# Performance work log

Measured on AMD Instinct MI355X. Metric: run time of the kernel, lower is better.

Reference implementation:

```python
import jax, jax.numpy as jnp
import numpy as np

B, T, N, F, H, K, E = 4, 256, 48, 4, 64, 4, 192
LH, C = 512, 8
NEG_SLOPE = 0.2


def setup_inputs() -> dict:
    key = jax.random.key(0)
    ks = jax.random.split(key, 16)
    rn = lambda k, shape, s=0.1: jax.random.normal(k, shape, jnp.float32) * s
    x = jax.random.normal(ks[0], (B, T, N, F), jnp.float32)
    edge_index = jax.random.randint(ks[1], (2, E), 0, N, jnp.int32)
    return dict(
        x=x,
        edge_index=edge_index,
        # GATv2 layer 1: F -> K*H, concat heads
        Wl1=rn(ks[2], (F, K * H)), Wr1=rn(ks[3], (F, K * H)),
        att1=rn(ks[4], (K, H)), b1=rn(ks[5], (K * H,)),
        # GATv2 layer 2: K*H -> H, mean over heads
        Wl2=rn(ks[6], (K * H, K * H)), Wr2=rn(ks[7], (K * H, K * H)),
        att2=rn(ks[8], (K, H)), b2=rn(ks[9], (H,)),
        # LSTM (torch gate order i,f,g,o)
        W_ih=rn(ks[10], (4 * LH, N * H), 0.02), W_hh=rn(ks[11], (4 * LH, LH), 0.02),
        b_ih=rn(ks[12], (4 * LH,), 0.02), b_hh=rn(ks[13], (4 * LH,), 0.02),
        fc_w=rn(ks[14], (C, LH)), fc_b=rn(ks[15], (C,)),
    )


def gatv2(xn, src, dst, Wl, Wr, att, bias, concat):
    # xn: [G, N, Fin]; shared edge list src/dst: [E]
    G = xn.shape[0]
    xl = (xn @ Wl).reshape(G, N, K, H)  # source transform (messages)
    xr = (xn @ Wr).reshape(G, N, K, H)  # target transform
    s = jax.nn.leaky_relu(xl[:, src] + xr[:, dst], NEG_SLOPE)  # [G,E,K,H]
    e = jnp.einsum('gekh,kh->gek', s, att)                      # [G,E,K]
    seg_max = jax.vmap(lambda v: jax.ops.segment_max(v, dst, num_segments=N))(e)  # [G,N,K]
    p = jnp.exp(e - seg_max[:, dst])
    denom = jax.vmap(lambda v: jax.ops.segment_sum(v, dst, num_segments=N))(p)
    alpha = p / (denom[:, dst] + 1e-16)                         # softmax over in-edges per node
    msg = alpha[..., None] * xl[:, src]                         # [G,E,K,H]
    out = jax.vmap(lambda m: jax.ops.segment_sum(m, dst, num_segments=N))(msg)  # [G,N,K,H]
    out = out.reshape(G, N, K * H) if concat else out.mean(axis=2)
    return out + bias


def lstm_last(seq, W_ih, W_hh, b_ih, b_hh):
    # seq: [B, T, In] -> last hidden state [B, LH]
    xw = jnp.einsum('bti,gi->btg', seq, W_ih) + (b_ih + b_hh)  # precompute input part
    def step(carry, xt):
        h, c = carry
        g = xt + h @ W_hh.T
        i, f, gg, o = jnp.split(g, 4, axis=-1)
        c = jax.nn.sigmoid(f) * c + jax.nn.sigmoid(i) * jnp.tanh(gg)
        h = jax.nn.sigmoid(o) * jnp.tanh(c)
        return (h, c), None
    h0 = jnp.zeros((seq.shape[0], LH), seq.dtype)
    (h, _c), _ = jax.lax.scan(step, (h0, h0), jnp.swapaxes(xw, 0, 1))
    return h


def reference(x, edge_index, Wl1, Wr1, att1, b1, Wl2, Wr2, att2, b2,
              W_ih, W_hh, b_ih, b_hh, fc_w, fc_b):
    src, dst = edge_index[0], edge_index[1]
    xg = x.reshape(B * T, N, F)
    h1 = jax.nn.relu(gatv2(xg, src, dst, Wl1, Wr1, att1, b1, True))   # [G,N,K*H]
    h2 = jax.nn.relu(gatv2(h1, src, dst, Wl2, Wr2, att2, b2, False))  # [G,N,H]
    seq = h2.reshape(B, T, N * H)
    hT = lstm_last(seq, W_ih, W_hh, b_ih, b_hh)
    return hT @ fc_w.T + fc_b  # [B, C]
```

## Files before the change

kernel.cpp:

```cpp
#include <hip/hip_runtime.h>
#include <math.h>

typedef unsigned short u16;
typedef unsigned int u32;
typedef unsigned long long u64;

#define NB 4
#define NT 256
#define NN 48
#define NF 4
#define NH 64
#define NK 4
#define NE 192
#define NLH 512
#define NC 8
#define NG 1024
#define KH 256
#define SEQD 3072
#define G4 2048
#define LSTM_NBLK 64
#define XS 520

typedef __attribute__((ext_vector_type(8))) short bf16x8;
typedef __attribute__((ext_vector_type(4))) float f32x4;

__device__ __forceinline__ float bf2f(u16 v) {
  union { u32 u; float f; } c; c.u = ((u32)v) << 16; return c.f;
}
__device__ __forceinline__ u16 f2bf(float f) {
  union { float f; u32 u; } c; c.f = f;
  u32 r = c.u + 0x7FFFu + ((c.u >> 16) & 1u);
  return (u16)(r >> 16);
}
__device__ __forceinline__ u32 fbits(float f) { union { float f; u32 u; } c; c.f = f; return c.u; }
__device__ __forceinline__ float bitsf(u32 u) { union { u32 u; float f; } c; c.u = u; return c.f; }

__device__ __forceinline__ float sigm_fast(float x) {
  return 1.f / (1.f + __expf(-x));
}
__device__ __forceinline__ float tanh_fast(float x) {
  float ax = fabsf(x);
  float t = __expf(-2.f * ax);
  float r = (1.f - t) / (1.f + t);
  return x < 0.f ? -r : r;
}

__global__ void setup_kernel(const int* __restrict__ ei, int* __restrict__ coff,
                             int* __restrict__ ceid)
{
  __shared__ int sdst[NE];
  __shared__ int scnt[NN + 1];
  const int tid = threadIdx.x;
  for (int e = tid; e < NE; e += 64) sdst[e] = ei[NE + e];
  if (tid < NN + 1) scnt[tid] = 0;
  __syncthreads();
  if (tid < NN) {
    int c = 0;
    for (int e = 0; e < NE; ++e) c += (sdst[e] == tid) ? 1 : 0;
    scnt[tid + 1] = c;
  }
  __syncthreads();
  if (tid == 0) {
    int acc = 0;
    coff[0] = 0;
#pragma unroll
    for (int n = 0; n < NN; ++n) {
      acc += scnt[n + 1];
      scnt[n + 1] = acc;
      coff[n + 1] = acc;
    }
  }
  __syncthreads();
  if (tid < NN) {
    int p = scnt[tid];
    for (int e = 0; e < NE; ++e)
      if (sdst[e] == tid) ceid[p++] = e;
  }
}

__global__ void wtc_kernel(const float* __restrict__ Wl2, const float* __restrict__ Wr2,
                           u16* __restrict__ WTc)
{
  int id0 = blockIdx.x * 256 + threadIdx.x;
#pragma unroll
  for (int rep = 0; rep < 4; ++rep) {
    int id = id0 + rep * 32768;
    int n = id >> 8, k = id & 255;
    float v = (n < 256) ? Wl2[k * 256 + n] : Wr2[k * 256 + (n - 256)];
    WTc[id] = f2bf(v);
  }
}

__global__ void wihb_kernel(const float* __restrict__ Wih, u16* __restrict__ WihB)
{
  int id = (blockIdx.x * 256 + threadIdx.x) * 8;
  float4 a = *(const float4*)(Wih + id);
  float4 b = *(const float4*)(Wih + id + 4);
  u16* dst = WihB + id;
  dst[0] = f2bf(a.x); dst[1] = f2bf(a.y); dst[2] = f2bf(a.z); dst[3] = f2bf(a.w);
  dst[4] = f2bf(b.x); dst[5] = f2bf(b.y); dst[6] = f2bf(b.z); dst[7] = f2bf(b.w);
}

__global__ __launch_bounds__(256) void gat_fused_kernel(
    const float* __restrict__ x, const int* __restrict__ ei,
    const int* __restrict__ coff, const int* __restrict__ ceid,
    const float* __restrict__ Wl1, const float* __restrict__ Wr1,
    const float* __restrict__ att1, const float* __restrict__ b1,
    const u16* __restrict__ WTc,
    const float* __restrict__ att2, const float* __restrict__ b2,
    u16* __restrict__ h2b)
{
  __shared__ __attribute__((aligned(16))) u16 xlds[NN * XS];
  __shared__ float sWl1[NF * KH], sWr1[NF * KH];
  __shared__ float satt[KH];
  __shared__ float sbias[KH];
  __shared__ float sx[NN * NF];
  __shared__ float esc[NE * NK];
  __shared__ int soff[NN + 1];
  __shared__ u16 seid[NE], ssrc[NE], sdst[NE];

  const int tid = threadIdx.x;
  const int g = blockIdx.x;
  const int lane = tid & 63, wv = tid >> 6;
  const int l15 = lane & 15, q = lane >> 4;

#pragma unroll
  for (int rep = 0; rep < 4; ++rep) {
    int idx = rep * 256 + tid;
    sWl1[idx] = Wl1[idx];
    sWr1[idx] = Wr1[idx];
  }
  satt[tid] = att1[tid];
  sbias[tid] = b1[tid];
  if (tid < NN * NF) sx[tid] = x[(size_t)g * (NN * NF) + tid];
  if (tid < NE) {
    ssrc[tid] = (u16)ei[tid];
    sdst[tid] = (u16)ei[NE + tid];
    seid[tid] = (u16)ceid[tid];
  }
  if (tid < NN + 1) soff[tid] = coff[tid];
  __syncthreads();

  {
    float w0 = sWl1[tid], w1 = sWl1[256 + tid], w2 = sWl1[512 + tid], w3 = sWl1[768 + tid];
    float v0 = sWr1[tid], v1 = sWr1[256 + tid], v2 = sWr1[512 + tid], v3 = sWr1[768 + tid];
#pragma unroll 4
    for (int n = 0; n < NN; ++n) {
      float x0 = sx[n * 4 + 0], x1 = sx[n * 4 + 1], x2 = sx[n * 4 + 2], x3 = sx[n * 4 + 3];
      float xl = fmaf(x3, w3, fmaf(x2, w2, fmaf(x1, w1, x0 * w0)));
      float xr = fmaf(x3, v3, fmaf(x2, v2, fmaf(x1, v1, x0 * v0)));
      xlds[n * XS + tid] = f2bf(xl);
      xlds[n * XS + 256 + tid] = f2bf(xr);
    }
  }
  __syncthreads();

  for (int e = tid; e < NE; e += 256) {
    int s = ssrc[e], d = sdst[e];
    const u16* xls = xlds + s * XS;
    const u16* xrd = xlds + d * XS + 256;
#pragma unroll
    for (int k = 0; k < 4; ++k) {
      float acc = 0.f;
#pragma unroll
      for (int c = 0; c < 8; ++c) {
        bf16x8 av = *(const bf16x8*)(xls + k * 64 + c * 8);
        bf16x8 bv = *(const bf16x8*)(xrd + k * 64 + c * 8);
        const float* ap = satt + k * 64 + c * 8;
#pragma unroll
        for (int j = 0; j < 8; ++j) {
          float tv = bf2f((u16)av[j]) + bf2f((u16)bv[j]);
          tv = tv > 0.f ? tv : 0.2f * tv;
          acc = fmaf(tv, ap[j], acc);
        }
      }
      esc[e * 4 + k] = acc;
    }
  }
  __syncthreads();

  if (tid < NN * NK) {
    int n = tid >> 2, k = tid & 3;
    int e0 = soff[n], e1 = soff[n + 1];
    if (e1 > e0) {
      float m = -1e30f;
      for (int j = e0; j < e1; ++j) m = fmaxf(m, esc[seid[j] * 4 + k]);
      float den = 0.f;
      for (int j = e0; j < e1; ++j) {
        float pv = expf(esc[seid[j] * 4 + k] - m);
        esc[seid[j] * 4 + k] = pv;
        den += pv;
      }
      float inv = 1.f / (den + 1e-16f);
      for (int j = e0; j < e1; ++j) esc[seid[j] * 4 + k] *= inv;
    }
  }
  __syncthreads();

  satt[tid] = att2[tid];
  {
    int o = tid, k = o >> 6;
    for (int n = 0; n < NN; ++n) {
      int e0 = soff[n], e1 = soff[n + 1];
      float acc = 0.f;
      for (int j = e0; j < e1; ++j) {
        int e = seid[j];
        int s = ssrc[e];
        acc = fmaf(esc[e * 4 + k], bf2f(xlds[s * XS + o]), acc);
      }
      float ov = acc + sbias[o];
      xlds[n * XS + 256 + o] = f2bf(fmaxf(ov, 0.f));
    }
  }
  __syncthreads();
  if (tid < NH) sbias[tid] = b2[tid];

  bf16x8 afr[3][8];
#pragma unroll
  for (int mt = 0; mt < 3; ++mt)
#pragma unroll
    for (int kt = 0; kt < 8; ++kt)
      afr[mt][kt] = *(const bf16x8*)(xlds + (mt * 16 + l15) * XS + 256 + kt * 32 + q * 8);
  __syncthreads();

#pragma unroll
  for (int t = 0; t < 8; ++t) {
    int n0 = (wv * 8 + t) * 16;
    const u16* bcol = WTc + (size_t)(n0 + l15) * KH + q * 8;
    f32x4 acc0 = {0.f, 0.f, 0.f, 0.f}, acc1 = acc0, acc2 = acc0;
#pragma unroll
    for (int kt = 0; kt < 8; ++kt) {
      bf16x8 bfr = *(const bf16x8*)(bcol + kt * 32);
      acc0 = __builtin_amdgcn_mfma_f32_16x16x32_bf16(afr[0][kt], bfr, acc0, 0, 0, 0);
      acc1 = __builtin_amdgcn_mfma_f32_16x16x32_bf16(afr[1][kt], bfr, acc1, 0, 0, 0);
      acc2 = __builtin_amdgcn_mfma_f32_16x16x32_bf16(afr[2][kt], bfr, acc2, 0, 0, 0);
    }
#pragma unroll
    for (int r = 0; r < 4; ++r) {
      int rw = q * 4 + r;
      xlds[(0 * 16 + rw) * XS + n0 + l15] = f2bf(acc0[r]);
      xlds[(1 * 16 + rw) * XS + n0 + l15] = f2bf(acc1[r]);
      xlds[(2 * 16 + rw) * XS + n0 + l15] = f2bf(acc2[r]);
    }
  }
  __syncthreads();

  for (int e = tid; e < NE; e += 256) {
    int s = ssrc[e], d = sdst[e];
    const u16* xls = xlds + s * XS;
    const u16* xrd = xlds + d * XS + 256;
#pragma unroll
    for (int k = 0; k < 4; ++k) {
      float acc = 0.f;
#pragma unroll
      for (int c = 0; c < 8; ++c) {
        bf16x8 av = *(const bf16x8*)(xls + k * 64 + c * 8);
        bf16x8 bv = *(const bf16x8*)(xrd + k * 64 + c * 8);
        const float* ap = satt + k * 64 + c * 8;
#pragma unroll
        for (int j = 0; j < 8; ++j) {
          float tv = bf2f((u16)av[j]) + bf2f((u16)bv[j]);
          tv = tv > 0.f ? tv : 0.2f * tv;
          acc = fmaf(tv, ap[j], acc);
        }
      }
      esc[e * 4 + k] = acc;
    }
  }
  __syncthreads();

  if (tid < NN * NK) {
    int n = tid >> 2, k = tid & 3;
    int e0 = soff[n], e1 = soff[n + 1];
    if (e1 > e0) {
      float m = -1e30f;
      for (int j = e0; j < e1; ++j) m = fmaxf(m, esc[seid[j] * 4 + k]);
      float den = 0.f;
      for (int j = e0; j < e1; ++j) {
        float pv = expf(esc[seid[j] * 4 + k] - m);
        esc[seid[j] * 4 + k] = pv;
        den += pv;
      }
      float inv = 1.f / (den + 1e-16f);
      for (int j = e0; j < e1; ++j) esc[seid[j] * 4 + k] *= inv;
    }
  }
  __syncthreads();

  for (int task = tid; task < NN * NH; task += 256) {
    int n = task >> 6, h = task & 63;
    int e0 = soff[n], e1 = soff[n + 1];
    float acc = 0.f;
    for (int j = e0; j < e1; ++j) {
      int e = seid[j];
      int s = ssrc[e];
      const u16* xls = xlds + s * XS + h;
#pragma unroll
      for (int k = 0; k < 4; ++k)
        acc = fmaf(esc[e * 4 + k], bf2f(xls[k * 64]), acc);
    }
    float ov = fmaf(acc, 0.25f, sbias[h]);
    h2b[(size_t)g * SEQD + task] = f2bf(fmaxf(ov, 0.f));
  }
}

__global__ __launch_bounds__(256) void xw_mfma_kernel(const u16* __restrict__ h2b,
                                                      const u16* __restrict__ WihB,
                                                      const float* __restrict__ bih,
                                                      const float* __restrict__ bhh,
                                                      float* __restrict__ xw)
{
  const int tid = threadIdx.x, lane = tid & 63, wv = tid >> 6;
  const int l15 = lane & 15, q = lane >> 4;
  const int gt = blockIdx.x & 15, rt = blockIdx.x >> 4;
  const int g0 = gt * 64, r0 = rt * 128;

  const u16* arow[4];
#pragma unroll
  for (int mt = 0; mt < 4; ++mt)
    arow[mt] = h2b + (size_t)(g0 + mt * 16 + l15) * SEQD + q * 8;
  const u16* brow[2];
  int ncol[2];
#pragma unroll
  for (int tn = 0; tn < 2; ++tn) {
    ncol[tn] = r0 + (wv * 2 + tn) * 16 + l15;
    brow[tn] = WihB + (size_t)ncol[tn] * SEQD + q * 8;
  }

  f32x4 acc[4][2];
#pragma unroll
  for (int mt = 0; mt < 4; ++mt)
#pragma unroll
    for (int tn = 0; tn < 2; ++tn) acc[mt][tn] = (f32x4){0.f, 0.f, 0.f, 0.f};

  for (int kt = 0; kt < SEQD / 32; ++kt) {
    bf16x8 af[4], bfv[2];
#pragma unroll
    for (int mt = 0; mt < 4; ++mt) af[mt] = *(const bf16x8*)(arow[mt] + kt * 32);
#pragma unroll
    for (int tn = 0; tn < 2; ++tn) bfv[tn] = *(const bf16x8*)(brow[tn] + kt * 32);
#pragma unroll
    for (int mt = 0; mt < 4; ++mt)
#pragma unroll
      for (int tn = 0; tn < 2; ++tn)
        acc[mt][tn] = __builtin_amdgcn_mfma_f32_16x16x32_bf16(af[mt], bfv[tn], acc[mt][tn], 0, 0, 0);
  }

#pragma unroll
  for (int tn = 0; tn < 2; ++tn) {
    float bias = bih[ncol[tn]] + bhh[ncol[tn]];
#pragma unroll
    for (int mt = 0; mt < 4; ++mt)
#pragma unroll
      for (int r = 0; r < 4; ++r) {
        int gg = g0 + mt * 16 + q * 4 + r;
        xw[(size_t)gg * G4 + ncol[tn]] = acc[mt][tn][r] + bias;
      }
  }
}

__global__ __launch_bounds__(256) void lstm_kernel(const float* __restrict__ xw,
                                                   const float* __restrict__ Whh,
                                                   const float* __restrict__ fcw,
                                                   const float* __restrict__ fcb,
                                                   u64* pairs,
                                                   float* __restrict__ out)
{
  __shared__ float hlds[NB * NLH];
  __shared__ float part[2][8][32][4];
  __shared__ float clds[8][4];
  __shared__ float fcpart[32][8];

  const int tid = threadIdx.x;
  const int blk = blockIdx.x;
  const int r32 = tid & 31, p = tid >> 5;
  const int lane = tid & 63, w = tid >> 6;
  const int R = (r32 >> 3) * NLH + blk * 8 + (r32 & 7);

  float wreg[64];
  {
    const float4* wsrc = (const float4*)(Whh + (size_t)R * NLH + p * 64);
#pragma unroll
    for (int q = 0; q < 16; ++q) {
      float4 v = wsrc[q];
      wreg[4 * q + 0] = v.x; wreg[4 * q + 1] = v.y;
      wreg[4 * q + 2] = v.z; wreg[4 * q + 3] = v.w;
    }
  }
  if (tid < 32) {
    int u = tid & 7, b = tid >> 3;
    clds[u][b] = 0.f;
    __hip_atomic_store(&pairs[0 * (NB * NLH) + b * NLH + blk * 8 + u], 0ULL,
                       __ATOMIC_RELAXED, __HIP_MEMORY_SCOPE_AGENT);
  }

  for (int s = 0; s < NT; ++s) {
    float myxw[4];
    if (tid < 32) {
      int u = tid & 7, b = tid >> 3;
#pragma unroll
      for (int G = 0; G < 4; ++G)
        myxw[G] = xw[(size_t)(b * NT + s) * G4 + G * 512 + blk * 8 + u];
    }
    {
      u64* pb = pairs + (size_t)(s & 1) * (NB * NLH);
      const int u0 = w * 128 + lane, u1 = u0 + 64;
      u64 v[8];
      while (true) {
#pragma unroll
        for (int b = 0; b < NB; ++b) {
          v[2 * b]     = __hip_atomic_load(&pb[b * NLH + u0],
                                           __ATOMIC_RELAXED, __HIP_MEMORY_SCOPE_AGENT);
          v[2 * b + 1] = __hip_atomic_load(&pb[b * NLH + u1],
                                           __ATOMIC_RELAXED, __HIP_MEMORY_SCOPE_AGENT);
        }
        int mn = 0x7fffffff;
#pragma unroll
        for (int q = 0; q < 8; ++q) mn = min(mn, (int)(u32)(v[q] >> 32));
        if (__all(mn >= s)) break;
      }
#pragma unroll
      for (int b = 0; b < NB; ++b) {
        hlds[b * NLH + u0] = bitsf((u32)v[2 * b]);
        hlds[b * NLH + u1] = bitsf((u32)v[2 * b + 1]);
      }
    }

    float a0 = 0.f, a1 = 0.f, a2 = 0.f, a3 = 0.f;
    const float* h0 = &hlds[0 * NLH + p * 64];
    const float* h1p = &hlds[1 * NLH + p * 64];
    const float* h2p = &hlds[2 * NLH + p * 64];
    const float* h3p = &hlds[3 * NLH + p * 64];
#pragma unroll
    for (int j = 0; j < 16; ++j) {
      float w0 = wreg[4 * j], w1 = wreg[4 * j + 1], w2 = wreg[4 * j + 2], w3 = wreg[4 * j + 3];
      float4 v0 = *(const float4*)(h0 + 4 * j);
      float4 v1 = *(const float4*)(h1p + 4 * j);
      float4 v2 = *(const float4*)(h2p + 4 * j);
      float4 v3 = *(const float4*)(h3p + 4 * j);
      a0 = fmaf(v0.w, w3, fmaf(v0.z, w2, fmaf(v0.y, w1, fmaf(v0.x, w0, a0))));
      a1 = fmaf(v1.w, w3, fmaf(v1.z, w2, fmaf(v1.y, w1, fmaf(v1.x, w0, a1))));
      a2 = fmaf(v2.w, w3, fmaf(v2.z, w2, fmaf(v2.y, w1, fmaf(v2.x, w0, a2))));
      a3 = fmaf(v3.w, w3, fmaf(v3.z, w2, fmaf(v3.y, w1, fmaf(v3.x, w0, a3))));
    }
    float (*pt)[32][4] = part[s & 1];
    pt[p][r32][0] = a0; pt[p][r32][1] = a1;
    pt[p][r32][2] = a2; pt[p][r32][3] = a3;
    __syncthreads();
    if (tid < 32) {
      int u = tid & 7, b = tid >> 3;
      float gsum[4];
#pragma unroll
      for (int G = 0; G < 4; ++G) {
        float t = myxw[G];
#pragma unroll
        for (int pp = 0; pp < 8; ++pp) t += pt[pp][G * 8 + u][b];
        gsum[G] = t;
      }
      float si = sigm_fast(gsum[0]);
      float sf = sigm_fast(gsum[1]);
      float so = sigm_fast(gsum[3]);
      float cn = fmaf(sf, clds[u][b], si * tanh_fast(gsum[2]));
      float hn = so * tanh_fast(cn);
      clds[u][b] = cn;
      u64 pk = ((u64)(u32)(s + 1) << 32) | (u64)fbits(hn);
      __hip_atomic_store(&pairs[(size_t)((s + 1) & 1) * (NB * NLH) + b * NLH + blk * 8 + u],
                         pk, __ATOMIC_RELAXED, __HIP_MEMORY_SCOPE_AGENT);
    }
  }

  if (blk == 0) {
    {
      u64* pb = pairs + (size_t)(NT & 1) * (NB * NLH);
      const int u0 = w * 128 + lane, u1 = u0 + 64;
      u64 v[8];
      while (true) {
#pragma unroll
        for (int b = 0; b < NB; ++b) {
          v[2 * b]     = __hip_atomic_load(&pb[b * NLH + u0],
                                           __ATOMIC_RELAXED, __HIP_MEMORY_SCOPE_AGENT);
          v[2 * b + 1] = __hip_atomic_load(&pb[b * NLH + u1],
                                           __ATOMIC_RELAXED, __HIP_MEMORY_SCOPE_AGENT);
        }
        int mn = 0x7fffffff;
#pragma unroll
        for (int q = 0; q < 8; ++q) mn = min(mn, (int)(u32)(v[q] >> 32));
        if (__all(mn >= NT)) break;
      }
#pragma unroll
      for (int b = 0; b < NB; ++b) {
        hlds[b * NLH + u0] = bitsf((u32)v[2 * b]);
        hlds[b * NLH + u1] = bitsf((u32)v[2 * b + 1]);
      }
    }
    __syncthreads();
    int pr = tid >> 3, l = tid & 7;
    int b = pr >> 3, cc = pr & 7;
    const float* hf = hlds + b * NLH;
    float a = 0.f;
    int base = cc * NLH + l * 64;
    for (int j = 0; j < 64; ++j) a = fmaf(hf[l * 64 + j], fcw[base + j], a);
    fcpart[pr][l] = a;
    __syncthreads();
    if (tid < 32) {
      float s = fcb[tid & 7];
#pragma unroll
      for (int l2 = 0; l2 < 8; ++l2) s += fcpart[tid][l2];
      out[tid] = s;
    }
  }
}

extern "C" void kernel_launch(void* const* d_in, const int* in_sizes, int n_in,
                              void* d_out, int out_size, void* d_ws, size_t ws_size,
                              hipStream_t stream)
{
  (void)in_sizes; (void)n_in; (void)out_size; (void)ws_size;
  const float* x    = (const float*)d_in[0];
  const int*   ei   = (const int*)d_in[1];
  const float* Wl1  = (const float*)d_in[2];
  const float* Wr1  = (const float*)d_in[3];
  const float* att1 = (const float*)d_in[4];
  const float* b1   = (const float*)d_in[5];
  const float* Wl2  = (const float*)d_in[6];
  const float* Wr2  = (const float*)d_in[7];
  const float* att2 = (const float*)d_in[8];
  const float* b2   = (const float*)d_in[9];
  const float* Wih  = (const float*)d_in[10];
  const float* Whh  = (const float*)d_in[11];
  const float* bih  = (const float*)d_in[12];
  const float* bhh  = (const float*)d_in[13];
  const float* fcw  = (const float*)d_in[14];
  const float* fcb  = (const float*)d_in[15];

  char* ws = (char*)d_ws;
  int* csr_off = (int*)(ws + 0);
  int* csr_eid = (int*)(ws + 256);
  u64* pairs   = (u64*)(ws + 1024);
  u16* WTc     = (u16*)(ws + 40960);
  u16* WihB    = (u16*)(ws + 303104);
  u16* h2b     = (u16*)(ws + 12886016);
  float* xwb   = (float*)(ws + 19177472);
  float* outp  = (float*)d_out;

  setup_kernel<<<1, 64, 0, stream>>>(ei, csr_off, csr_eid);
  wtc_kernel<<<128, 256, 0, stream>>>(Wl2, Wr2, WTc);
  wihb_kernel<<<3072, 256, 0, stream>>>(Wih, WihB);
  gat_fused_kernel<<<NG, 256, 0, stream>>>(x, ei, csr_off, csr_eid,
                                           Wl1, Wr1, att1, b1,
                                           WTc, att2, b2, h2b);
  xw_mfma_kernel<<<256, 256, 0, stream>>>(h2b, WihB, bih, bhh, xwb);
  lstm_kernel<<<LSTM_NBLK, 256, 0, stream>>>(xwb, Whh, fcw, fcb, pairs, outp);
}
```

Measured before the change: 1.171 ms.

## Store attention scores in CSR order and flatten per-node aggregation loops

The setup kernel now also writes CSR-ordered source ids, destination node ids, last-edge flags and an edge-to-slot map. The GAT kernel writes edge scores directly into CSR slots, which removes the seid indirection in the softmax and aggregation. Both aggregations become a single flat loop over all edges that flushes a node's result at its last edge, instead of a per-node loop with data-dependent bounds. Layer 2 splits the nodes into four groups of twelve per wave, so each wave scans all 192 edges but computes only its own group, and nodes with no in-edges are patched separately. The cost is extra shared memory and redundant edge scanning in layer 2.

New measurement: 1.189 ms. Within noise of the previous version (+1.5%).

```diff
diff --git a/kernel.cpp b/kernel.cpp
--- a/kernel.cpp
+++ b/kernel.cpp
@@ -46,12 +46,16 @@
 }
 
 __global__ void setup_kernel(const int* __restrict__ ei, int* __restrict__ coff,
-                             int* __restrict__ ceid)
-{
-  __shared__ int sdst[NE];
+                             int* __restrict__ ceid, int* __restrict__ aux)
+{
+  __shared__ int sdst[NE], ssrcs[NE];
   __shared__ int scnt[NN + 1];
   const int tid = threadIdx.x;
-  for (int e = tid; e < NE; e += 64) sdst[e] = ei[NE + e];
+  for (int e = tid; e < NE; e += 64) {
+    ssrcs[e] = ei[e];
+    sdst[e] = ei[NE + e];
+    aux[2 * NE + e] = 0;
+  }
   if (tid < NN + 1) scnt[tid] = 0;
   __syncthreads();
   if (tid < NN) {
@@ -72,9 +76,16 @@
   }
   __syncthreads();
   if (tid < NN) {
-    int p = scnt[tid];
+    int p0 = scnt[tid], p = p0;
     for (int e = 0; e < NE; ++e)
-      if (sdst[e] == tid) ceid[p++] = e;
+      if (sdst[e] == tid) {
+        ceid[p] = e;
+        aux[p] = ssrcs[e];
+        aux[NE + p] = tid;
+        aux[3 * NE + e] = p;
+        ++p;
+      }
+    if (p > p0) aux[2 * NE + p - 1] = 1;
   }
 }
 
@@ -103,7 +114,7 @@
 
 __global__ __launch_bounds__(256) void gat_fused_kernel(
     const float* __restrict__ x, const int* __restrict__ ei,
-    const int* __restrict__ coff, const int* __restrict__ ceid,
+    const int* __restrict__ coff, const int* __restrict__ aux,
     const float* __restrict__ Wl1, const float* __restrict__ Wr1,
     const float* __restrict__ att1, const float* __restrict__ b1,
     const u16* __restrict__ WTc,
@@ -115,9 +126,10 @@
   __shared__ float satt[KH];
   __shared__ float sbias[KH];
   __shared__ float sx[NN * NF];
-  __shared__ float esc[NE * NK];
+  __shared__ float escC[NE * NK];
   __shared__ int soff[NN + 1];
-  __shared__ u16 seid[NE], ssrc[NE], sdst[NE];
+  __shared__ u16 ssrc[NE], sdst[NE];
+  __shared__ u16 scsrc[NE], snode[NE], slast[NE], sepos[NE];
 
   const int tid = threadIdx.x;
   const int g = blockIdx.x;
@@ -136,7 +148,10 @@
   if (tid < NE) {
     ssrc[tid] = (u16)ei[tid];
     sdst[tid] = (u16)ei[NE + tid];
-    seid[tid] = (u16)ceid[tid];
+    scsrc[tid] = (u16)aux[tid];
+    snode[tid] = (u16)aux[NE + tid];
+    slast[tid] = (u16)aux[2 * NE + tid];
+    sepos[tid] = (u16)aux[3 * NE + tid];
   }
   if (tid < NN + 1) soff[tid] = coff[tid];
   __syncthreads();
@@ -157,6 +172,7 @@
 
   for (int e = tid; e < NE; e += 256) {
     int s = ssrc[e], d = sdst[e];
+    int slot = sepos[e];
     const u16* xls = xlds + s * XS;
     const u16* xrd = xlds + d * XS + 256;
 #pragma unroll
@@ -174,7 +190,7 @@
           acc = fmaf(tv, ap[j], acc);
         }
       }
-      esc[e * 4 + k] = acc;
+      escC[slot * 4 + k] = acc;
     }
   }
   __syncthreads();
@@ -184,33 +200,36 @@
     int e0 = soff[n], e1 = soff[n + 1];
     if (e1 > e0) {
       float m = -1e30f;
-      for (int j = e0; j < e1; ++j) m = fmaxf(m, esc[seid[j] * 4 + k]);
+      for (int j = e0; j < e1; ++j) m = fmaxf(m, escC[j * 4 + k]);
       float den = 0.f;
       for (int j = e0; j < e1; ++j) {
-        float pv = expf(esc[seid[j] * 4 + k] - m);
-        esc[seid[j] * 4 + k] = pv;
+        float pv = expf(escC[j * 4 + k] - m);
+        escC[j * 4 + k] = pv;
         den += pv;
       }
       float inv = 1.f / (den + 1e-16f);
-      for (int j = e0; j < e1; ++j) esc[seid[j] * 4 + k] *= inv;
+      for (int j = e0; j < e1; ++j) escC[j * 4 + k] *= inv;
     }
   }
   __syncthreads();
 
   satt[tid] = att2[tid];
   {
-    int o = tid, k = o >> 6;
-    for (int n = 0; n < NN; ++n) {
-      int e0 = soff[n], e1 = soff[n + 1];
-      float acc = 0.f;
-      for (int j = e0; j < e1; ++j) {
-        int e = seid[j];
-        int s = ssrc[e];
-        acc = fmaf(esc[e * 4 + k], bf2f(xlds[s * XS + o]), acc);
-      }
-      float ov = acc + sbias[o];
-      xlds[n * XS + 256 + o] = f2bf(fmaxf(ov, 0.f));
-    }
+    const int o = tid, k = o >> 6;
+    float acc = 0.f;
+#pragma unroll 4
+    for (int j = 0; j < NE; ++j) {
+      int src = scsrc[j];
+      acc = fmaf(escC[j * 4 + k], bf2f(xlds[src * XS + o]), acc);
+      if (slast[j]) {
+        int n = snode[j];
+        xlds[n * XS + 256 + o] = f2bf(fmaxf(acc + sbias[o], 0.f));
+        acc = 0.f;
+      }
+    }
+    for (int n = 0; n < NN; ++n)
+      if (soff[n + 1] == soff[n])
+        xlds[n * XS + 256 + o] = f2bf(fmaxf(sbias[o], 0.f));
   }
   __syncthreads();
   if (tid < NH) sbias[tid] = b2[tid];
@@ -247,6 +266,7 @@
 
   for (int e = tid; e < NE; e += 256) {
     int s = ssrc[e], d = sdst[e];
+    int slot = sepos[e];
     const u16* xls = xlds + s * XS;
     const u16* xrd = xlds + d * XS + 256;
 #pragma unroll
@@ -264,7 +284,7 @@
           acc = fmaf(tv, ap[j], acc);
         }
       }
-      esc[e * 4 + k] = acc;
+      escC[slot * 4 + k] = acc;
     }
   }
   __syncthreads();
@@ -274,33 +294,41 @@
     int e0 = soff[n], e1 = soff[n + 1];
     if (e1 > e0) {
       float m = -1e30f;
-      for (int j = e0; j < e1; ++j) m = fmaxf(m, esc[seid[j] * 4 + k]);
+      for (int j = e0; j < e1; ++j) m = fmaxf(m, escC[j * 4 + k]);
       float den = 0.f;
       for (int j = e0; j < e1; ++j) {
-        float pv = expf(esc[seid[j] * 4 + k] - m);
-        esc[seid[j] * 4 + k] = pv;
+        float pv = expf(escC[j * 4 + k] - m);
+        escC[j * 4 + k] = pv;
         den += pv;
       }
       float inv = 1.f / (den + 1e-16f);
-      for (int j = e0; j < e1; ++j) esc[seid[j] * 4 + k] *= inv;
-    }
-  }
-  __syncthreads();
-
-  for (int task = tid; task < NN * NH; task += 256) {
-    int n = task >> 6, h = task & 63;
-    int e0 = soff[n], e1 = soff[n + 1];
+      for (int j = e0; j < e1; ++j) escC[j * 4 + k] *= inv;
+    }
+  }
+  __syncthreads();
+
+  {
+    const int h = tid & 63, grp = tid >> 6;
+    const int nlo = grp * 12;
     float acc = 0.f;
-    for (int j = e0; j < e1; ++j) {
-      int e = seid[j];
-      int s = ssrc[e];
-      const u16* xls = xlds + s * XS + h;
-#pragma unroll
-      for (int k = 0; k < 4; ++k)
-        acc = fmaf(esc[e * 4 + k], bf2f(xls[k * 64]), acc);
-    }
-    float ov = fmaf(acc, 0.25f, sbias[h]);
-    h2b[(size_t)g * SEQD + task] = f2bf(fmaxf(ov, 0.f));
+#pragma unroll 4
+    for (int j = 0; j < NE; ++j) {
+      int n = snode[j];
+      if ((u32)(n - nlo) < 12u) {
+        int src = scsrc[j];
+        const u16* xls = xlds + src * XS + h;
+#pragma unroll
+        for (int k = 0; k < 4; ++k)
+          acc = fmaf(escC[j * 4 + k], bf2f(xls[k * 64]), acc);
+        if (slast[j]) {
+          h2b[(size_t)g * SEQD + n * 64 + h] = f2bf(fmaxf(fmaf(acc, 0.25f, sbias[h]), 0.f));
+          acc = 0.f;
+        }
+      }
+    }
+    for (int n = nlo; n < nlo + 12; ++n)
+      if (soff[n + 1] == soff[n])
+        h2b[(size_t)g * SEQD + n * 64 + h] = f2bf(fmaxf(sbias[h], 0.f));
   }
 }
 
@@ -537,16 +565,17 @@
   int* csr_off = (int*)(ws + 0);
   int* csr_eid = (int*)(ws + 256);
   u64* pairs   = (u64*)(ws + 1024);
+  int* csr_aux = (int*)(ws + 33792);
   u16* WTc     = (u16*)(ws + 40960);
   u16* WihB    = (u16*)(ws + 303104);
   u16* h2b     = (u16*)(ws + 12886016);
   float* xwb   = (float*)(ws + 19177472);
   float* outp  = (float*)d_out;
 
-  setup_kernel<<<1, 64, 0, stream>>>(ei, csr_off, csr_eid);
+  setup_kernel<<<1, 64, 0, stream>>>(ei, csr_off, csr_eid, csr_aux);
   wtc_kernel<<<128, 256, 0, stream>>>(Wl2, Wr2, WTc);
   wihb_kernel<<<3072, 256, 0, stream>>>(Wih, WihB);
-  gat_fused_kernel<<<NG, 256, 0, stream>>>(x, ei, csr_off, csr_eid,
+  gat_fused_kernel<<<NG, 256, 0, stream>>>(x, ei, csr_off, csr_aux,
                                            Wl1, Wr1, att1, b1,
                                            WTc, att2, b2, h2b);
   xw_mfma_kernel<<<256, 256, 0, stream>>>(h2b, WihB, bih, bhh, xwb);
```
